# Kernel tuning notes

Hardware: AMD Instinct MI355X
Metric: run time of the kernel (lower is better)

The kernel has to match this reference:

```python
import jax, jax.numpy as jnp
import numpy as np

BS, C, H, W = 8, 128, 64, 64
CH = C // 2  # proj output channels


def setup_inputs() -> dict:
    key = jax.random.key(0)
    ks = jax.random.split(key, 8)
    s = 1.0 / np.sqrt(C)
    return {
        "tgt": jax.random.normal(ks[0], (BS, C, H, W), dtype=jnp.float32),
        "ref": jax.random.normal(ks[1], (BS, C, H, W), dtype=jnp.float32),
        "W_tgt": jax.random.normal(ks[2], (CH, C), dtype=jnp.float32) * s,
        "b_tgt": jax.random.normal(ks[3], (CH,), dtype=jnp.float32) * s,
        "W_ref": jax.random.normal(ks[4], (CH, C), dtype=jnp.float32) * s,
        "b_ref": jax.random.normal(ks[5], (CH,), dtype=jnp.float32) * s,
        "W_out": jax.random.normal(ks[6], (C, C), dtype=jnp.float32) * s,
        "b_out": jax.random.normal(ks[7], (C,), dtype=jnp.float32) * s,
    }


def reference(tgt, ref, W_tgt, b_tgt, W_ref, b_ref, W_out, b_out):
    bs, c, h, w = tgt.shape
    n = h * w
    # 1x1 conv == per-pixel matmul over channels; flatten spatial to tokens
    tgt_f = tgt.reshape(bs, c, n)              # [bs, c, n]
    ref_f = ref.reshape(bs, c, n)              # [bs, c, n]
    # att_tgt: [bs, n, c/2] ; att_ref: [bs, c/2, n] (ReLU after proj)
    att_tgt = jax.nn.relu(jnp.einsum('bcn,oc->bno', tgt_f, W_tgt) + b_tgt)
    att_ref = jax.nn.relu(jnp.einsum('bcn,oc->bon', ref_f, W_ref) + b_ref[None, :, None])
    pre_att = jnp.einsum('bnd,bdm->bnm', att_tgt, att_ref)   # [bs, n, n]
    att = jax.nn.softmax(pre_att, axis=-1)
    # fused tokens: [bs, n, c] = att @ ref_tokens
    fused = jnp.einsum('bnm,bcm->bnc', att, ref_f)
    fused = fused.transpose(0, 2, 1).reshape(bs, c, h, w)
    # output gate: 1x1 conv on tgt (no activation), elementwise mul
    att_out = jnp.einsum('bcn,oc->bon', tgt_f, W_out) + b_out[None, :, None]
    fused = fused * att_out.reshape(bs, c, h, w)
    return fused
```

## Files before the change

kernel.cpp:

```cpp
#include <hip/hip_runtime.h>

typedef __attribute__((ext_vector_type(8))) _Float16 f16x8;
typedef __attribute__((ext_vector_type(4))) float f32x4;

constexpr int kC  = 128;
constexpr int kCH = 64;
constexpr int kN  = 4096;
constexpr float kLog2e = 1.4426950408889634f;

__device__ __forceinline__ unsigned pkrtz(float a, float b) {
    union { __fp16 __attribute__((ext_vector_type(2))) v; unsigned u; } cv;
    cv.v = __builtin_amdgcn_cvt_pkrtz(a, b);
    return cv.u;
}

__device__ __forceinline__ void g2l16(const unsigned short* g, unsigned short* l) {
    __builtin_amdgcn_global_load_lds(
        (const __attribute__((address_space(1))) unsigned int*)(g),
        (__attribute__((address_space(3))) unsigned int*)(l),
        16, 0, 0);
}

__global__ __launch_bounds__(256, 3) void proj_mfma(
    const float* __restrict__ tgt, const float* __restrict__ ref,
    const float* __restrict__ Wt, const float* __restrict__ Wr,
    const float* __restrict__ Wo, const float* __restrict__ bt,
    const float* __restrict__ br, const float* __restrict__ bo,
    unsigned short* __restrict__ Qw, unsigned short* __restrict__ Kw,
    unsigned short* __restrict__ Vw, float* __restrict__ Gw)
{
    __shared__ __align__(16) unsigned short Xs[128 * 128];
    const int t = threadIdx.x;
    const int slice = blockIdx.y >> 3;
    const int b = blockIdx.y & 7;
    const int tokb = blockIdx.x << 7;

    const float* X = (slice == 1) ? ref : tgt;
    const float* Xb = X + ((size_t)b * kC) * kN + tokb;
    unsigned short* Vout = Vw + ((size_t)b * kC) * kN + tokb;

    const int tk4 = (t & 31) * 4;
    const int c8a = (t >> 5) * 8;
    #pragma unroll
    for (int half = 0; half < 2; ++half) {
        const int c8 = c8a + half * 64;
        f32x4 xv[8];
        #pragma unroll
        for (int j = 0; j < 8; ++j)
            xv[j] = *(const f32x4*)(Xb + (size_t)(c8 + j) * kN + tk4);
        if (slice == 1) {
            #pragma unroll
            for (int j = 0; j < 8; ++j)
                *(uint2*)(Vout + (size_t)(c8 + j) * kN + tk4) =
                    make_uint2(pkrtz(xv[j][0], xv[j][1]), pkrtz(xv[j][2], xv[j][3]));
        }
        #pragma unroll
        for (int s = 0; s < 4; ++s) {
            const int tok = tk4 + s;
            const int cc = (c8 >> 3) ^ (tok & 7);
            uint4 pk;
            pk.x = pkrtz(xv[0][s], xv[1][s]);
            pk.y = pkrtz(xv[2][s], xv[3][s]);
            pk.z = pkrtz(xv[4][s], xv[5][s]);
            pk.w = pkrtz(xv[6][s], xv[7][s]);
            *(uint4*)(Xs + tok * 128 + cc * 8) = pk;
        }
    }
    __syncthreads();

    const int w = t >> 6, lane = t & 63;
    const int lg = (lane >> 4) & 3, lm = lane & 15;

    if (slice == 2) {
        const int ocb = w * 32;
        f16x8 wf[2][4];
        float bvv[2][4];
        #pragma unroll
        for (int ot = 0; ot < 2; ++ot) {
            const int oc = ocb + ot * 16 + lm;
            #pragma unroll
            for (int ks = 0; ks < 4; ++ks) {
                const float* wp = Wo + (size_t)oc * kC + ks * 32 + lg * 8;
                f32x4 f0 = *(const f32x4*)wp;
                f32x4 f1 = *(const f32x4*)(wp + 4);
                union { f16x8 h; uint4 u; } cv;
                cv.u = make_uint4(pkrtz(f0[0], f0[1]), pkrtz(f0[2], f0[3]),
                                  pkrtz(f1[0], f1[1]), pkrtz(f1[2], f1[3]));
                wf[ot][ks] = cv.h;
            }
            #pragma unroll
            for (int r = 0; r < 4; ++r) bvv[ot][r] = bo[ocb + ot * 16 + lg * 4 + r];
        }

        float* Gb = Gw + ((size_t)b * kC) * kN + tokb;
        #pragma unroll
        for (int ns = 0; ns < 8; ++ns) {
            const int tok = ns * 16 + lm;
            f16x8 xf[4];
            #pragma unroll
            for (int ks = 0; ks < 4; ++ks)
                xf[ks] = *(const f16x8*)(Xs + tok * 128 +
                                         (((ks * 4 + lg) ^ (tok & 7)) << 3));
            #pragma unroll
            for (int ot = 0; ot < 2; ++ot) {
                f32x4 acc = {bvv[ot][0], bvv[ot][1], bvv[ot][2], bvv[ot][3]};
                #pragma unroll
                for (int ks = 0; ks < 4; ++ks)
                    acc = __builtin_amdgcn_mfma_f32_16x16x32_f16(wf[ot][ks], xf[ks], acc, 0, 0, 0);
                #pragma unroll
                for (int r = 0; r < 4; ++r)
                    Gb[(size_t)(ocb + ot * 16 + lg * 4 + r) * kN + tok] = acc[r];
            }
        }
    } else {
        const float* W    = slice ? Wr : Wt;
        const float* bias = slice ? br : bt;
        const float scale = slice ? 1.0f : kLog2e;
        const int ocb = w * 16;

        f16x8 wf[4];
        #pragma unroll
        for (int ks = 0; ks < 4; ++ks) {
            const float* wp = W + (size_t)(ocb + lm) * kC + ks * 32 + lg * 8;
            f32x4 f0 = *(const f32x4*)wp;
            f32x4 f1 = *(const f32x4*)(wp + 4);
            union { f16x8 h; uint4 u; } cv;
            cv.u = make_uint4(pkrtz(f0[0] * scale, f0[1] * scale),
                              pkrtz(f0[2] * scale, f0[3] * scale),
                              pkrtz(f1[0] * scale, f1[1] * scale),
                              pkrtz(f1[2] * scale, f1[3] * scale));
            wf[ks] = cv.h;
        }
        float bv[4];
        #pragma unroll
        for (int r = 0; r < 4; ++r) bv[r] = bias[ocb + lg * 4 + r] * scale;

        unsigned short* outp = (slice ? Kw : Qw) + ((size_t)b * kN + tokb) * kCH;
        #pragma unroll
        for (int ns = 0; ns < 8; ++ns) {
            const int tok = ns * 16 + lm;
            f16x8 xf[4];
            #pragma unroll
            for (int ks = 0; ks < 4; ++ks)
                xf[ks] = *(const f16x8*)(Xs + tok * 128 +
                                         (((ks * 4 + lg) ^ (tok & 7)) << 3));
            f32x4 acc = {bv[0], bv[1], bv[2], bv[3]};
            #pragma unroll
            for (int ks = 0; ks < 4; ++ks)
                acc = __builtin_amdgcn_mfma_f32_16x16x32_f16(wf[ks], xf[ks], acc, 0, 0, 0);
            uint2 pk;
            pk.x = pkrtz(fmaxf(acc[0], 0.f), fmaxf(acc[1], 0.f));
            pk.y = pkrtz(fmaxf(acc[2], 0.f), fmaxf(acc[3], 0.f));
            *(uint2*)(outp + (size_t)tok * kCH + ocb + lg * 4) = pk;
        }
    }
}

__global__ __launch_bounds__(256, 2) void flash6_kernel(
    const unsigned short* __restrict__ Qw,
    const unsigned short* __restrict__ Kw,
    const unsigned short* __restrict__ Vw,
    const float* __restrict__ Gw,
    float* __restrict__ out)
{
    __shared__ __align__(16) unsigned short Ks[2][64 * 64];
    __shared__ __align__(16) unsigned short Vs[2][128 * 64];
    __shared__ __align__(16) unsigned short Ps[64 * 64];

    const int t = threadIdx.x;
    const int b = blockIdx.x & 7;
    const int n0 = (blockIdx.x >> 3) << 6;
    const int w = t >> 6, lane = t & 63;
    const int lg = (lane >> 4) & 3, lm = lane & 15;
    const int row_q = w * 16 + lm;
    const int swz = lm & 7;

    const unsigned short* Qb = Qw + ((size_t)b * kN) * kCH;
    const unsigned short* Kb = Kw + ((size_t)b * kN) * kCH;
    const unsigned short* Vb = Vw + ((size_t)b * kC) * kN;

    f16x8 qf0 = *(const f16x8*)(Qb + (size_t)(n0 + row_q) * kCH + (lg << 3));
    f16x8 qf1 = *(const f16x8*)(Qb + (size_t)(n0 + row_q) * kCH + 32 + (lg << 3));

    const int srow = t >> 3, scol = t & 7;
    const int sco  = (scol ^ (srow & 7)) << 3;
    const int wv   = t >> 6;

    const int fswz0 = (lg ^ swz) << 3;
    const int fswz1 = ((4 | lg) ^ swz) << 3;
    int psw[4];
    #pragma unroll
    for (int mb = 0; mb < 4; ++mb)
        psw[mb] = row_q * 64 + (((2 * mb + (lg >> 1)) ^ swz) << 3) + ((lg & 1) << 2);

    union { f16x8 h; uint4 u; } onec;
    onec.u = make_uint4(0x3c003c00u, 0x3c003c00u, 0x3c003c00u, 0x3c003c00u);
    const f16x8 onev = onec.h;

    f32x4 O[8];
    #pragma unroll
    for (int cb = 0; cb < 8; ++cb) O[cb] = (f32x4){0.f, 0.f, 0.f, 0.f};
    f32x4 L = (f32x4){0.f, 0.f, 0.f, 0.f};
    float m_run = 0.0f;

    auto stage = [&](int buf, int m0) {
        g2l16(Kb + (size_t)(m0 + srow) * kCH + sco,      Ks[buf] + wv * 512);
        g2l16(Kb + (size_t)(m0 + 32 + srow) * kCH + sco, Ks[buf] + 2048 + wv * 512);
        #pragma unroll
        for (int j = 0; j < 4; ++j)
            g2l16(Vb + (size_t)(32 * j + srow) * kN + m0 + sco,
                  Vs[buf] + j * 2048 + wv * 512);
    };
    stage(0, 0);

    for (int kt = 0; kt < kN / 64; ++kt) {
        const int cur = kt & 1;
        __syncthreads();
        if (kt + 1 < kN / 64) stage(cur ^ 1, (kt + 1) << 6);

        f32x4 s[4];
        __builtin_amdgcn_s_setprio(1);
        #pragma unroll
        for (int mb = 0; mb < 4; ++mb) {
            const unsigned short* kr = Ks[cur] + ((mb * 16 + lm) << 6);
            f16x8 kf0 = *(const f16x8*)(kr + fswz0);
            f16x8 kf1 = *(const f16x8*)(kr + fswz1);
            f32x4 acc = (f32x4){0.f, 0.f, 0.f, 0.f};
            acc = __builtin_amdgcn_mfma_f32_16x16x32_f16(kf0, qf0, acc, 0, 0, 0);
            acc = __builtin_amdgcn_mfma_f32_16x16x32_f16(kf1, qf1, acc, 0, 0, 0);
            s[mb] = acc;
        }
        __builtin_amdgcn_s_setprio(0);

        float mloc = 0.0f;
        #pragma unroll
        for (int mb = 0; mb < 4; ++mb)
            #pragma unroll
            for (int r = 0; r < 4; ++r) mloc = fmaxf(mloc, s[mb][r]);
        mloc = fmaxf(mloc, __shfl_xor(mloc, 16, 64));
        mloc = fmaxf(mloc, __shfl_xor(mloc, 32, 64));
        const bool upd = __any(mloc > m_run);
        const float mnew = upd ? fmaxf(m_run, mloc) : m_run;

        #pragma unroll
        for (int mb = 0; mb < 4; ++mb) {
            unsigned plo = pkrtz(exp2f(s[mb][0] - mnew), exp2f(s[mb][1] - mnew));
            unsigned phi = pkrtz(exp2f(s[mb][2] - mnew), exp2f(s[mb][3] - mnew));
            *(uint2*)(Ps + psw[mb]) = make_uint2(plo, phi);
        }

        if (upd) {
            float alpha = exp2f(m_run - mnew);
            float a0 = __shfl(alpha, (lg << 2) + 0, 64);
            float a1 = __shfl(alpha, (lg << 2) + 1, 64);
            float a2 = __shfl(alpha, (lg << 2) + 2, 64);
            float a3 = __shfl(alpha, (lg << 2) + 3, 64);
            #pragma unroll
            for (int cb = 0; cb < 8; ++cb) {
                O[cb][0] *= a0; O[cb][1] *= a1; O[cb][2] *= a2; O[cb][3] *= a3;
            }
            L[0] *= a0; L[1] *= a1; L[2] *= a2; L[3] *= a3;
            m_run = mnew;
        }

        f16x8 pf0 = *(const f16x8*)(Ps + row_q * 64 + fswz0);
        f16x8 pf1 = *(const f16x8*)(Ps + row_q * 64 + fswz1);
        __builtin_amdgcn_s_setprio(1);
        L = __builtin_amdgcn_mfma_f32_16x16x32_f16(pf0, onev, L, 0, 0, 0);
        L = __builtin_amdgcn_mfma_f32_16x16x32_f16(pf1, onev, L, 0, 0, 0);
        #pragma unroll
        for (int cb = 0; cb < 8; ++cb) {
            const unsigned short* vr = Vs[cur] + ((cb * 16 + lm) << 6);
            f16x8 vf0 = *(const f16x8*)(vr + fswz0);
            f16x8 vf1 = *(const f16x8*)(vr + fswz1);
            O[cb] = __builtin_amdgcn_mfma_f32_16x16x32_f16(pf0, vf0, O[cb], 0, 0, 0);
            O[cb] = __builtin_amdgcn_mfma_f32_16x16x32_f16(pf1, vf1, O[cb], 0, 0, 0);
        }
        __builtin_amdgcn_s_setprio(0);
    }

    const float i0 = 1.0f / L[0], i1 = 1.0f / L[1];
    const float i2 = 1.0f / L[2], i3 = 1.0f / L[3];
    const float* Gb = Gw + ((size_t)b * kC) * kN;
    float* Ob = out + ((size_t)b * kC) * kN;
    #pragma unroll
    for (int cb = 0; cb < 8; ++cb) {
        int c = cb * 16 + lm;
        size_t base = (size_t)c * kN + n0 + w * 16 + (lg << 2);
        float4 g = *(const float4*)(Gb + base);
        float4 res;
        res.x = O[cb][0] * i0 * g.x;
        res.y = O[cb][1] * i1 * g.y;
        res.z = O[cb][2] * i2 * g.z;
        res.w = O[cb][3] * i3 * g.w;
        *(float4*)(Ob + base) = res;
    }
}

extern "C" void kernel_launch(void* const* d_in, const int* in_sizes, int n_in,
                              void* d_out, int out_size, void* d_ws, size_t ws_size,
                              hipStream_t stream) {
    const float* tgt   = (const float*)d_in[0];
    const float* ref   = (const float*)d_in[1];
    const float* W_tgt = (const float*)d_in[2];
    const float* b_tgt = (const float*)d_in[3];
    const float* W_ref = (const float*)d_in[4];
    const float* b_ref = (const float*)d_in[5];
    const float* W_out = (const float*)d_in[6];
    const float* b_out = (const float*)d_in[7];
    float* out = (float*)d_out;

    const size_t QK = (size_t)8 * kN * kCH;
    const size_t CV = (size_t)8 * kC * kN;
    unsigned short* Qw = (unsigned short*)d_ws;
    unsigned short* Kw = Qw + QK;
    unsigned short* Vw = Kw + QK;
    float*          Gw = (float*)(Vw + CV);

    proj_mfma<<<dim3(32, 24), 256, 0, stream>>>(tgt, ref, W_tgt, W_ref, W_out,
                                                b_tgt, b_ref, b_out, Qw, Kw, Vw, Gw);
    flash6_kernel<<<dim3(512), 256, 0, stream>>>(Qw, Kw, Vw, Gw, out);
}
```

Baseline: 195.4 us.

## Halve projection tiles, hoist weight loads before sync, unroll attention double-buffer loop

The projection kernel now processes 64 tokens per block instead of 128, which doubles the grid and shrinks shared memory so more blocks fit per CU. Weight and bias loads are issued before the LDS staging and barrier so they overlap with the input loads. The flash kernel's main loop is unrolled by two with buffer pointers passed explicitly, removing runtime buffer indexing. exp2f is replaced with the raw hardware exp2 builtin, which skips the range-handling wrapper and may differ slightly on denormals.

New measurement: 186.8 us. 4.4% less time.

```diff
diff --git a/kernel.cpp b/kernel.cpp
--- a/kernel.cpp
+++ b/kernel.cpp
@@ -12,6 +12,10 @@
     union { __fp16 __attribute__((ext_vector_type(2))) v; unsigned u; } cv;
     cv.v = __builtin_amdgcn_cvt_pkrtz(a, b);
     return cv.u;
+}
+
+__device__ __forceinline__ float x2(float x) {
+    return __builtin_amdgcn_exp2f(x);
 }
 
 __device__ __forceinline__ void g2l16(const unsigned short* g, unsigned short* l) {
@@ -21,7 +25,7 @@
         16, 0, 0);
 }
 
-__global__ __launch_bounds__(256, 3) void proj_mfma(
+__global__ __launch_bounds__(256, 4) void proj_mfma(
     const float* __restrict__ tgt, const float* __restrict__ ref,
     const float* __restrict__ Wt, const float* __restrict__ Wr,
     const float* __restrict__ Wo, const float* __restrict__ bt,
@@ -29,52 +33,30 @@
     unsigned short* __restrict__ Qw, unsigned short* __restrict__ Kw,
     unsigned short* __restrict__ Vw, float* __restrict__ Gw)
 {
-    __shared__ __align__(16) unsigned short Xs[128 * 128];
+    __shared__ __align__(16) unsigned short Xs[64 * 128];
     const int t = threadIdx.x;
     const int slice = blockIdx.y >> 3;
     const int b = blockIdx.y & 7;
-    const int tokb = blockIdx.x << 7;
+    const int tokb = blockIdx.x << 6;
+
+    const int w = t >> 6, lane = t & 63;
+    const int lg = (lane >> 4) & 3, lm = lane & 15;
 
     const float* X = (slice == 1) ? ref : tgt;
     const float* Xb = X + ((size_t)b * kC) * kN + tokb;
     unsigned short* Vout = Vw + ((size_t)b * kC) * kN + tokb;
 
-    const int tk4 = (t & 31) * 4;
-    const int c8a = (t >> 5) * 8;
-    #pragma unroll
-    for (int half = 0; half < 2; ++half) {
-        const int c8 = c8a + half * 64;
-        f32x4 xv[8];
-        #pragma unroll
-        for (int j = 0; j < 8; ++j)
-            xv[j] = *(const f32x4*)(Xb + (size_t)(c8 + j) * kN + tk4);
-        if (slice == 1) {
-            #pragma unroll
-            for (int j = 0; j < 8; ++j)
-                *(uint2*)(Vout + (size_t)(c8 + j) * kN + tk4) =
-                    make_uint2(pkrtz(xv[j][0], xv[j][1]), pkrtz(xv[j][2], xv[j][3]));
-        }
-        #pragma unroll
-        for (int s = 0; s < 4; ++s) {
-            const int tok = tk4 + s;
-            const int cc = (c8 >> 3) ^ (tok & 7);
-            uint4 pk;
-            pk.x = pkrtz(xv[0][s], xv[1][s]);
-            pk.y = pkrtz(xv[2][s], xv[3][s]);
-            pk.z = pkrtz(xv[4][s], xv[5][s]);
-            pk.w = pkrtz(xv[6][s], xv[7][s]);
-            *(uint4*)(Xs + tok * 128 + cc * 8) = pk;
-        }
-    }
-    __syncthreads();
-
-    const int w = t >> 6, lane = t & 63;
-    const int lg = (lane >> 4) & 3, lm = lane & 15;
-
+    const int tk4 = (t & 15) * 4;
+    const int c8  = (t >> 4) * 8;
+    f32x4 xv[8];
+    #pragma unroll
+    for (int j = 0; j < 8; ++j)
+        xv[j] = *(const f32x4*)(Xb + (size_t)(c8 + j) * kN + tk4);
+
+    f16x8 wf[2][4];
+    float bvv[2][4];
     if (slice == 2) {
         const int ocb = w * 32;
-        f16x8 wf[2][4];
-        float bvv[2][4];
         #pragma unroll
         for (int ot = 0; ot < 2; ++ot) {
             const int oc = ocb + ot * 16 + lm;
@@ -91,10 +73,51 @@
             #pragma unroll
             for (int r = 0; r < 4; ++r) bvv[ot][r] = bo[ocb + ot * 16 + lg * 4 + r];
         }
-
+    } else {
+        const float* W    = slice ? Wr : Wt;
+        const float* bias = slice ? br : bt;
+        const float scale = slice ? 1.0f : kLog2e;
+        const int ocb = w * 16;
+        #pragma unroll
+        for (int ks = 0; ks < 4; ++ks) {
+            const float* wp = W + (size_t)(ocb + lm) * kC + ks * 32 + lg * 8;
+            f32x4 f0 = *(const f32x4*)wp;
+            f32x4 f1 = *(const f32x4*)(wp + 4);
+            union { f16x8 h; uint4 u; } cv;
+            cv.u = make_uint4(pkrtz(f0[0] * scale, f0[1] * scale),
+                              pkrtz(f0[2] * scale, f0[3] * scale),
+                              pkrtz(f1[0] * scale, f1[1] * scale),
+                              pkrtz(f1[2] * scale, f1[3] * scale));
+            wf[0][ks] = cv.h;
+        }
+        #pragma unroll
+        for (int r = 0; r < 4; ++r) bvv[0][r] = bias[ocb + lg * 4 + r] * scale;
+    }
+
+    if (slice == 1) {
+        #pragma unroll
+        for (int j = 0; j < 8; ++j)
+            *(uint2*)(Vout + (size_t)(c8 + j) * kN + tk4) =
+                make_uint2(pkrtz(xv[j][0], xv[j][1]), pkrtz(xv[j][2], xv[j][3]));
+    }
+    #pragma unroll
+    for (int s = 0; s < 4; ++s) {
+        const int tok = tk4 + s;
+        const int cc = (c8 >> 3) ^ (tok & 7);
+        uint4 pk;
+        pk.x = pkrtz(xv[0][s], xv[1][s]);
+        pk.y = pkrtz(xv[2][s], xv[3][s]);
+        pk.z = pkrtz(xv[4][s], xv[5][s]);
+        pk.w = pkrtz(xv[6][s], xv[7][s]);
+        *(uint4*)(Xs + tok * 128 + cc * 8) = pk;
+    }
+    __syncthreads();
+
+    if (slice == 2) {
+        const int ocb = w * 32;
         float* Gb = Gw + ((size_t)b * kC) * kN + tokb;
         #pragma unroll
-        for (int ns = 0; ns < 8; ++ns) {
+        for (int ns = 0; ns < 4; ++ns) {
             const int tok = ns * 16 + lm;
             f16x8 xf[4];
             #pragma unroll
@@ -113,41 +136,20 @@
             }
         }
     } else {
-        const float* W    = slice ? Wr : Wt;
-        const float* bias = slice ? br : bt;
-        const float scale = slice ? 1.0f : kLog2e;
         const int ocb = w * 16;
-
-        f16x8 wf[4];
-        #pragma unroll
-        for (int ks = 0; ks < 4; ++ks) {
-            const float* wp = W + (size_t)(ocb + lm) * kC + ks * 32 + lg * 8;
-            f32x4 f0 = *(const f32x4*)wp;
-            f32x4 f1 = *(const f32x4*)(wp + 4);
-            union { f16x8 h; uint4 u; } cv;
-            cv.u = make_uint4(pkrtz(f0[0] * scale, f0[1] * scale),
-                              pkrtz(f0[2] * scale, f0[3] * scale),
-                              pkrtz(f1[0] * scale, f1[1] * scale),
-                              pkrtz(f1[2] * scale, f1[3] * scale));
-            wf[ks] = cv.h;
-        }
-        float bv[4];
-        #pragma unroll
-        for (int r = 0; r < 4; ++r) bv[r] = bias[ocb + lg * 4 + r] * scale;
-
         unsigned short* outp = (slice ? Kw : Qw) + ((size_t)b * kN + tokb) * kCH;
         #pragma unroll
-        for (int ns = 0; ns < 8; ++ns) {
+        for (int ns = 0; ns < 4; ++ns) {
             const int tok = ns * 16 + lm;
             f16x8 xf[4];
             #pragma unroll
             for (int ks = 0; ks < 4; ++ks)
                 xf[ks] = *(const f16x8*)(Xs + tok * 128 +
                                          (((ks * 4 + lg) ^ (tok & 7)) << 3));
-            f32x4 acc = {bv[0], bv[1], bv[2], bv[3]};
+            f32x4 acc = {bvv[0][0], bvv[0][1], bvv[0][2], bvv[0][3]};
             #pragma unroll
             for (int ks = 0; ks < 4; ++ks)
-                acc = __builtin_amdgcn_mfma_f32_16x16x32_f16(wf[ks], xf[ks], acc, 0, 0, 0);
+                acc = __builtin_amdgcn_mfma_f32_16x16x32_f16(wf[0][ks], xf[ks], acc, 0, 0, 0);
             uint2 pk;
             pk.x = pkrtz(fmaxf(acc[0], 0.f), fmaxf(acc[1], 0.f));
             pk.y = pkrtz(fmaxf(acc[2], 0.f), fmaxf(acc[3], 0.f));
@@ -156,7 +158,7 @@
     }
 }
 
-__global__ __launch_bounds__(256, 2) void flash6_kernel(
+__global__ __launch_bounds__(256, 2) void flash7_kernel(
     const unsigned short* __restrict__ Qw,
     const unsigned short* __restrict__ Kw,
     const unsigned short* __restrict__ Vw,
@@ -203,26 +205,29 @@
     f32x4 L = (f32x4){0.f, 0.f, 0.f, 0.f};
     float m_run = 0.0f;
 
-    auto stage = [&](int buf, int m0) {
-        g2l16(Kb + (size_t)(m0 + srow) * kCH + sco,      Ks[buf] + wv * 512);
-        g2l16(Kb + (size_t)(m0 + 32 + srow) * kCH + sco, Ks[buf] + 2048 + wv * 512);
+    unsigned short* Ks0 = Ks[0]; unsigned short* Ks1 = Ks[1];
+    unsigned short* Vs0 = Vs[0]; unsigned short* Vs1 = Vs[1];
+
+    auto stage = [&](unsigned short* Kd, unsigned short* Vd, int m0) {
+        g2l16(Kb + (size_t)(m0 + srow) * kCH + sco,      Kd + wv * 512);
+        g2l16(Kb + (size_t)(m0 + 32 + srow) * kCH + sco, Kd + 2048 + wv * 512);
         #pragma unroll
         for (int j = 0; j < 4; ++j)
             g2l16(Vb + (size_t)(32 * j + srow) * kN + m0 + sco,
-                  Vs[buf] + j * 2048 + wv * 512);
+                  Vd + j * 2048 + wv * 512);
     };
-    stage(0, 0);
-
-    for (int kt = 0; kt < kN / 64; ++kt) {
-        const int cur = kt & 1;
+    stage(Ks0, Vs0, 0);
+
+    auto tile = [&](const unsigned short* Kc, const unsigned short* Vc,
+                    unsigned short* Kn, unsigned short* Vn, int kt) {
         __syncthreads();
-        if (kt + 1 < kN / 64) stage(cur ^ 1, (kt + 1) << 6);
+        if (kt + 1 < kN / 64) stage(Kn, Vn, (kt + 1) << 6);
 
         f32x4 s[4];
         __builtin_amdgcn_s_setprio(1);
         #pragma unroll
         for (int mb = 0; mb < 4; ++mb) {
-            const unsigned short* kr = Ks[cur] + ((mb * 16 + lm) << 6);
+            const unsigned short* kr = Kc + ((mb * 16 + lm) << 6);
             f16x8 kf0 = *(const f16x8*)(kr + fswz0);
             f16x8 kf1 = *(const f16x8*)(kr + fswz1);
             f32x4 acc = (f32x4){0.f, 0.f, 0.f, 0.f};
@@ -244,13 +249,13 @@
 
         #pragma unroll
         for (int mb = 0; mb < 4; ++mb) {
-            unsigned plo = pkrtz(exp2f(s[mb][0] - mnew), exp2f(s[mb][1] - mnew));
-            unsigned phi = pkrtz(exp2f(s[mb][2] - mnew), exp2f(s[mb][3] - mnew));
+            unsigned plo = pkrtz(x2(s[mb][0] - mnew), x2(s[mb][1] - mnew));
+            unsigned phi = pkrtz(x2(s[mb][2] - mnew), x2(s[mb][3] - mnew));
             *(uint2*)(Ps + psw[mb]) = make_uint2(plo, phi);
         }
 
         if (upd) {
-            float alpha = exp2f(m_run - mnew);
+            float alpha = x2(m_run - mnew);
             float a0 = __shfl(alpha, (lg << 2) + 0, 64);
             float a1 = __shfl(alpha, (lg << 2) + 1, 64);
             float a2 = __shfl(alpha, (lg << 2) + 2, 64);
@@ -270,13 +275,18 @@
         L = __builtin_amdgcn_mfma_f32_16x16x32_f16(pf1, onev, L, 0, 0, 0);
         #pragma unroll
         for (int cb = 0; cb < 8; ++cb) {
-            const unsigned short* vr = Vs[cur] + ((cb * 16 + lm) << 6);
+            const unsigned short* vr = Vc + ((cb * 16 + lm) << 6);
             f16x8 vf0 = *(const f16x8*)(vr + fswz0);
             f16x8 vf1 = *(const f16x8*)(vr + fswz1);
             O[cb] = __builtin_amdgcn_mfma_f32_16x16x32_f16(pf0, vf0, O[cb], 0, 0, 0);
             O[cb] = __builtin_amdgcn_mfma_f32_16x16x32_f16(pf1, vf1, O[cb], 0, 0, 0);
         }
         __builtin_amdgcn_s_setprio(0);
+    };
+
+    for (int kt = 0; kt < kN / 64; kt += 2) {
+        tile(Ks0, Vs0, Ks1, Vs1, kt);
+        tile(Ks1, Vs1, Ks0, Vs0, kt + 1);
     }
 
     const float i0 = 1.0f / L[0], i1 = 1.0f / L[1];
@@ -317,7 +327,7 @@
     unsigned short* Vw = Kw + QK;
     float*          Gw = (float*)(Vw + CV);
 
-    proj_mfma<<<dim3(32, 24), 256, 0, stream>>>(tgt, ref, W_tgt, W_ref, W_out,
+    proj_mfma<<<dim3(64, 24), 256, 0, stream>>>(tgt, ref, W_tgt, W_ref, W_out,
                                                 b_tgt, b_ref, b_out, Qw, Kw, Vw, Gw);
-    flash6_kernel<<<dim3(512), 256, 0, stream>>>(Qw, Kw, Vw, Gw, out);
-}
+    flash7_kernel<<<dim3(512), 256, 0, stream>>>(Qw, Kw, Vw, Gw, out);
+}
```
